# Kernel optimization log

Hardware: AMD Instinct MI355X
Metric: run time of the kernel (lower is better)

## Reference

```python
import jax, jax.numpy as jnp
import numpy as np

B, S, E, H = 8, 2048, 512, 4
D = E // H


def setup_inputs() -> dict:
    key = jax.random.key(0)
    ks = jax.random.split(key, 9)
    std = 0.05  # keras 'normal' initializer default stddev
    return {
        "x": jax.random.normal(ks[0], (B, S, E), dtype=jnp.float32),
        "Wq": jax.random.normal(ks[1], (E, E), dtype=jnp.float32) * std,
        "Wk": jax.random.normal(ks[2], (E, E), dtype=jnp.float32) * std,
        "Wv": jax.random.normal(ks[3], (E, E), dtype=jnp.float32) * std,
        "Wepi": jax.random.normal(ks[4], (S, S), dtype=jnp.float32) * std,
        "bq": jax.random.normal(ks[5], (S, 1), dtype=jnp.float32) * std,
        "bk": jax.random.normal(ks[6], (S, 1), dtype=jnp.float32) * std,
        "bv": jax.random.normal(ks[7], (S, 1), dtype=jnp.float32) * std,
        "bo": jax.random.normal(ks[8], (S, 1), dtype=jnp.float32) * std,
    }


def reference(x, Wq, Wk, Wv, Wepi, bq, bk, bv, bo):
    b, s, e = x.shape
    # QKV projections; [S,1] biases broadcast across the feature dim
    q = x @ Wq + bq  # [B,S,E]
    k = x @ Wk + bk
    v = x @ Wv + bv
    # split heads -> [B,H,S,D]
    q = q.reshape(b, s, H, D).transpose(0, 2, 1, 3)
    k = k.reshape(b, s, H, D).transpose(0, 2, 1, 3)
    v = v.reshape(b, s, H, D).transpose(0, 2, 1, 3)
    # NOTE: source scales by sqrt(seq_length), not sqrt(head_dim)
    scale = 1.0 / np.sqrt(float(s)).astype(np.float32)
    scores = jnp.einsum("bhsd,bhtd->bhst", q, k) * scale  # [B,H,S,S]
    attn = jax.nn.softmax(scores, axis=-1)
    # epigenomic multiplicative mask applied AFTER softmax (broadcast [S,S])
    attn = attn * Wepi
    effect = jnp.einsum("bhst,bhtd->bhsd", attn, v)  # [B,H,S,D]
    effect = effect.transpose(0, 2, 1, 3).reshape(b, s, e) + bo
    # original returns attention in merged-batch layout [B*H, S, S]
    return effect, attn.reshape(b * H, s, s)
```

## Files before the change

kernel.cpp:

```cpp
#include <hip/hip_runtime.h>
#include <hip/hip_bf16.h>

constexpr int Bn = 8, Sn = 2048, En = 512, Hn = 4, Dn = 128;
constexpr int BHn = Bn * Hn;
constexpr int Mqkv = Bn * Sn;

typedef __attribute__((ext_vector_type(8))) short short8;
typedef __attribute__((ext_vector_type(4))) float f32x4;

__device__ __forceinline__ unsigned short f2bf(float f) {
  unsigned int u = __builtin_bit_cast(unsigned int, f);
  u += 0x7FFF + ((u >> 16) & 1);
  return (unsigned short)(u >> 16);
}

__device__ __forceinline__ void bar_pub() {
  asm volatile("s_waitcnt lgkmcnt(0)" ::: "memory");
  __builtin_amdgcn_s_barrier();
  asm volatile("" ::: "memory");
}

__global__ __launch_bounds__(256) void qkv_kernel(
    const float* __restrict__ x, const float* __restrict__ Wq,
    const float* __restrict__ Wk, const float* __restrict__ Wv,
    const float* __restrict__ bq, const float* __restrict__ bk,
    const float* __restrict__ bv, unsigned short* __restrict__ qkv) {
  const int z = blockIdx.z;
  const float* W = (z == 0) ? Wq : (z == 1 ? Wk : Wv);
  const float* bias = (z == 0) ? bq : (z == 1 ? bk : bv);
  unsigned short* out = qkv + (size_t)z * BHn * Sn * Dn;

  __shared__ unsigned short As[128][40];
  __shared__ unsigned short BsT[128][40];

  const int t = threadIdx.x;
  const int l = t & 63, w = t >> 6;
  const int wm = w >> 1, wn = w & 1;
  const int m0 = blockIdx.x * 128, n0 = blockIdx.y * 128;

  f32x4 acc[4][4] = {};

  for (int k0 = 0; k0 < En; k0 += 32) {
    __syncthreads();
#pragma unroll
    for (int i = 0; i < 4; ++i) {
      int idx = t + i * 256;
      int row = idx >> 3, c4 = (idx & 7) * 4;
      float4 v = *reinterpret_cast<const float4*>(&x[(size_t)(m0 + row) * En + k0 + c4]);
      ushort4 p;
      p.x = f2bf(v.x); p.y = f2bf(v.y); p.z = f2bf(v.z); p.w = f2bf(v.w);
      *reinterpret_cast<ushort4*>(&As[row][c4]) = p;
    }
#pragma unroll
    for (int i = 0; i < 4; ++i) {
      int idx = t + i * 256;
      int kk = idx >> 5, c4 = (idx & 31) * 4;
      float4 v = *reinterpret_cast<const float4*>(&W[(size_t)(k0 + kk) * En + n0 + c4]);
      BsT[c4 + 0][kk] = f2bf(v.x);
      BsT[c4 + 1][kk] = f2bf(v.y);
      BsT[c4 + 2][kk] = f2bf(v.z);
      BsT[c4 + 3][kk] = f2bf(v.w);
    }
    __syncthreads();

    const int koff = (l >> 4) * 8;
    short8 a[4], bfr[4];
#pragma unroll
    for (int m = 0; m < 4; ++m)
      a[m] = *reinterpret_cast<const short8*>(&As[wm * 64 + m * 16 + (l & 15)][koff]);
#pragma unroll
    for (int n = 0; n < 4; ++n)
      bfr[n] = *reinterpret_cast<const short8*>(&BsT[wn * 64 + n * 16 + (l & 15)][koff]);
#pragma unroll
    for (int m = 0; m < 4; ++m)
#pragma unroll
      for (int n = 0; n < 4; ++n)
        acc[m][n] = __builtin_amdgcn_mfma_f32_16x16x32_bf16(a[m], bfr[n], acc[m][n], 0, 0, 0);
  }

#pragma unroll
  for (int m = 0; m < 4; ++m)
#pragma unroll
    for (int n = 0; n < 4; ++n)
#pragma unroll
      for (int j = 0; j < 4; ++j) {
        int row = m0 + wm * 64 + m * 16 + (l >> 4) * 4 + j;
        int col = n0 + wn * 64 + n * 16 + (l & 15);
        int s = row & (Sn - 1);
        float v = acc[m][n][j] + bias[s];
        int b = row >> 11;
        int h = col >> 7, d = col & 127;
        out[(size_t)((b * Hn + h) * Sn + s) * Dn + d] = f2bf(v);
      }
}

__global__ __launch_bounds__(256) void vtrans_kernel(
    const unsigned short* __restrict__ v, unsigned short* __restrict__ vT) {
  const int s0 = blockIdx.x * 64, d0 = blockIdx.y * 64;
  const int bh = blockIdx.z;
  const unsigned short* vp = v + (size_t)bh * Sn * Dn;
  unsigned short* op = vT + (size_t)bh * Dn * Sn;
  __shared__ unsigned short Ls[64][72];
  const int t = threadIdx.x;
#pragma unroll
  for (int it = 0; it < 2; ++it) {
    int flat = t + it * 256;
    int r = flat >> 3, cc = flat & 7;
    *reinterpret_cast<short8*>(&Ls[r][cc * 8]) =
        *reinterpret_cast<const short8*>(&vp[(size_t)(s0 + r) * Dn + d0 + cc * 8]);
  }
  __syncthreads();
#pragma unroll
  for (int it = 0; it < 2; ++it) {
    int flat = t + it * 256;
    int d = flat >> 3, sc = flat & 7;
    short8 o;
#pragma unroll
    for (int jo = 0; jo < 8; ++jo) {
      int jj = (jo + sc) & 7;
      o[jj] = (short)Ls[sc * 8 + jj][d];
    }
    *reinterpret_cast<short8*>(&op[(size_t)(d0 + d) * Sn + s0 + sc * 8]) = o;
  }
}

__global__ __launch_bounds__(256, 2) void fused_attn3_kernel(
    const unsigned short* __restrict__ qkv, const unsigned short* __restrict__ vT,
    const float* __restrict__ Wepi, const float* __restrict__ bo,
    float* __restrict__ attn, float* __restrict__ effect) {
  const int bh = blockIdx.y;
  const int s0 = blockIdx.x * 64;
  const unsigned short* qp = qkv + (size_t)bh * Sn * Dn;
  const unsigned short* kp = qkv + (size_t)(BHn + bh) * Sn * Dn;
  const unsigned short* vt = vT + (size_t)bh * Dn * Sn;

  __shared__ unsigned short Kb[2][64 * 128];
  __shared__ unsigned short Vt[128 * 64];
  __shared__ unsigned short Ps[64 * 64];

  const int t = threadIdx.x, l = t & 63, w = t >> 6;
  const int g = l >> 4, i = l & 15;
  const float scale = 0.022097086912079608f;

  short8 aq[4];
#pragma unroll
  for (int ks = 0; ks < 4; ++ks)
    aq[ks] = *reinterpret_cast<const short8*>(
        &qp[(size_t)(s0 + w * 16 + i) * Dn + ks * 32 + g * 8]);

  int ksrc[4], kdst[4], vsrc[4], vdst[4];
#pragma unroll
  for (int it = 0; it < 4; ++it) {
    int flat = t + it * 256;
    int r = flat >> 4, cc = flat & 15;
    ksrc[it] = r * Dn + cc * 8;
    kdst[it] = r * 128 + ((cc ^ (r & 15)) << 3);
    int d = flat >> 3, ct = flat & 7;
    vsrc[it] = d * Sn + ct * 8;
    vdst[it] = d * 64 + ((ct ^ (d & 7)) << 3);
  }

  short8 kreg[4];
#pragma unroll
  for (int it = 0; it < 4; ++it)
    kreg[it] = *reinterpret_cast<const short8*>(&kp[ksrc[it]]);
#pragma unroll
  for (int it = 0; it < 4; ++it)
    *reinterpret_cast<short8*>(&Kb[0][kdst[it]]) = kreg[it];
#pragma unroll
  for (int it = 0; it < 4; ++it)
    kreg[it] = *reinterpret_cast<const short8*>(&kp[(size_t)64 * Dn + ksrc[it]]);
  bar_pub();

  float rs[4] = {0.f, 0.f, 0.f, 0.f};

  for (int kt = 0; kt < 32; ++kt) {
    const int b = kt & 1;
    f32x4 acc[4] = {};
    __builtin_amdgcn_s_setprio(1);
#pragma unroll
    for (int ks = 0; ks < 4; ++ks)
#pragma unroll
      for (int nf = 0; nf < 4; ++nf) {
        short8 bk = *reinterpret_cast<const short8*>(
            &Kb[b][(nf * 16 + i) * 128 + (((ks * 4 + g) ^ i) << 3)]);
        acc[nf] = __builtin_amdgcn_mfma_f32_16x16x32_bf16(aq[ks], bk, acc[nf], 0, 0, 0);
      }
    __builtin_amdgcn_s_setprio(0);
#pragma unroll
    for (int j = 0; j < 4; ++j)
      rs[j] += __expf(acc[0][j] * scale) + __expf(acc[1][j] * scale) +
               __expf(acc[2][j] * scale) + __expf(acc[3][j] * scale);
    if (kt < 31) {
#pragma unroll
      for (int it = 0; it < 4; ++it)
        *reinterpret_cast<short8*>(&Kb[b ^ 1][kdst[it]]) = kreg[it];
      if (kt < 30)
#pragma unroll
        for (int it = 0; it < 4; ++it)
          kreg[it] = *reinterpret_cast<const short8*>(
              &kp[(size_t)(kt + 2) * 64 * Dn + ksrc[it]]);
    }
    bar_pub();
  }

  float rinv[4];
#pragma unroll
  for (int j = 0; j < 4; ++j) {
    float s = rs[j];
    s += __shfl_xor(s, 1); s += __shfl_xor(s, 2);
    s += __shfl_xor(s, 4); s += __shfl_xor(s, 8);
    rinv[j] = 1.0f / s;
  }

  short8 vreg[4];
#pragma unroll
  for (int it = 0; it < 4; ++it) {
    kreg[it] = *reinterpret_cast<const short8*>(&kp[ksrc[it]]);
    vreg[it] = *reinterpret_cast<const short8*>(&vt[vsrc[it]]);
  }
#pragma unroll
  for (int it = 0; it < 4; ++it) {
    *reinterpret_cast<short8*>(&Kb[0][kdst[it]]) = kreg[it];
    *reinterpret_cast<short8*>(&Vt[vdst[it]]) = vreg[it];
  }
#pragma unroll
  for (int it = 0; it < 4; ++it) {
    kreg[it] = *reinterpret_cast<const short8*>(&kp[(size_t)64 * Dn + ksrc[it]]);
    vreg[it] = *reinterpret_cast<const short8*>(&vt[64 + vsrc[it]]);
  }
  const float* wbase = Wepi + (size_t)(s0 + w * 16 + g * 4) * Sn + i;
  float wr[4][4];
#pragma unroll
  for (int nf = 0; nf < 4; ++nf)
#pragma unroll
    for (int j = 0; j < 4; ++j)
      wr[nf][j] = wbase[(size_t)j * Sn + nf * 16];
  bar_pub();

  f32x4 pv[8] = {};
  float* attn_bh = attn + (size_t)bh * Sn * Sn;

  for (int kt = 0; kt < 32; ++kt) {
    const int b = kt & 1;
    const int t0 = kt * 64;
    f32x4 acc[4] = {};
    __builtin_amdgcn_s_setprio(1);
#pragma unroll
    for (int ks = 0; ks < 4; ++ks)
#pragma unroll
      for (int nf = 0; nf < 4; ++nf) {
        short8 bk = *reinterpret_cast<const short8*>(
            &Kb[b][(nf * 16 + i) * 128 + (((ks * 4 + g) ^ i) << 3)]);
        acc[nf] = __builtin_amdgcn_mfma_f32_16x16x32_bf16(aq[ks], bk, acc[nf], 0, 0, 0);
      }
    __builtin_amdgcn_s_setprio(0);

#pragma unroll
    for (int nf = 0; nf < 4; ++nf)
#pragma unroll
      for (int j = 0; j < 4; ++j) {
        const int row = w * 16 + g * 4 + j;
        const int col = nf * 16 + i;
        float pf = __expf(acc[nf][j] * scale) * rinv[j] * wr[nf][j];
        attn_bh[(size_t)(s0 + row) * Sn + t0 + col] = pf;
        Ps[row * 64 + ((((nf * 2 + (i >> 3)) ^ (row & 7)) << 3) | (i & 7))] = f2bf(pf);
      }
    if (kt < 31)
#pragma unroll
      for (int nf = 0; nf < 4; ++nf)
#pragma unroll
        for (int j = 0; j < 4; ++j)
          wr[nf][j] = wbase[(size_t)j * Sn + t0 + 64 + nf * 16];
    if (kt < 31)
#pragma unroll
      for (int it = 0; it < 4; ++it)
        *reinterpret_cast<short8*>(&Kb[b ^ 1][kdst[it]]) = kreg[it];
    bar_pub();

    __builtin_amdgcn_s_setprio(1);
#pragma unroll
    for (int ks2 = 0; ks2 < 2; ++ks2) {
      short8 pa = *reinterpret_cast<const short8*>(
          &Ps[(w * 16 + i) * 64 + (((ks2 * 4 + g) ^ (i & 7)) << 3)]);
#pragma unroll
      for (int nf2 = 0; nf2 < 8; ++nf2) {
        const int d = nf2 * 16 + i;
        short8 bv = *reinterpret_cast<const short8*>(
            &Vt[d * 64 + (((ks2 * 4 + g) ^ (i & 7)) << 3)]);
        pv[nf2] = __builtin_amdgcn_mfma_f32_16x16x32_bf16(pa, bv, pv[nf2], 0, 0, 0);
      }
    }
    __builtin_amdgcn_s_setprio(0);
    bar_pub();

    if (kt < 31) {
#pragma unroll
      for (int it = 0; it < 4; ++it)
        *reinterpret_cast<short8*>(&Vt[vdst[it]]) = vreg[it];
      if (kt < 30)
#pragma unroll
        for (int it = 0; it < 4; ++it) {
          kreg[it] = *reinterpret_cast<const short8*>(
              &kp[(size_t)(t0 + 128) * Dn + ksrc[it]]);
          vreg[it] = *reinterpret_cast<const short8*>(&vt[t0 + 128 + vsrc[it]]);
        }
    }
  }

  const int b_ = bh >> 2, h_ = bh & 3;
#pragma unroll
  for (int j = 0; j < 4; ++j) {
    const int row = s0 + w * 16 + g * 4 + j;
    const float bias = bo[row];
#pragma unroll
    for (int nf2 = 0; nf2 < 8; ++nf2)
      effect[(size_t)(b_ * Sn + row) * En + h_ * Dn + nf2 * 16 + i] = pv[nf2][j] + bias;
  }
}

extern "C" void kernel_launch(void* const* d_in, const int* in_sizes, int n_in,
                              void* d_out, int out_size, void* d_ws, size_t ws_size,
                              hipStream_t stream) {
  const float* x    = (const float*)d_in[0];
  const float* Wq   = (const float*)d_in[1];
  const float* Wk   = (const float*)d_in[2];
  const float* Wv   = (const float*)d_in[3];
  const float* Wepi = (const float*)d_in[4];
  const float* bq   = (const float*)d_in[5];
  const float* bk   = (const float*)d_in[6];
  const float* bv   = (const float*)d_in[7];
  const float* bo   = (const float*)d_in[8];

  float* effect = (float*)d_out;
  float* attn = effect + (size_t)Bn * Sn * En;
  unsigned short* qkv = (unsigned short*)d_ws;
  unsigned short* vT = qkv + (size_t)3 * BHn * Sn * Dn;

  qkv_kernel<<<dim3(Mqkv / 128, En / 128, 3), 256, 0, stream>>>(x, Wq, Wk, Wv, bq, bk, bv, qkv);
  vtrans_kernel<<<dim3(Sn / 64, Dn / 64, BHn), 256, 0, stream>>>(
      qkv + (size_t)2 * BHn * Sn * Dn, vT);
  fused_attn3_kernel<<<dim3(Sn / 64, BHn), 256, 0, stream>>>(qkv, vT, Wepi, bo, attn, effect);
}
```

Before: 398.4 us.

## Transpose QK^T MFMA output for vectorized attn stores and per-wave P tiles

Swaps the MFMA operands so each lane holds four consecutive key columns of one query row. The attention probabilities and the Wepi mask can then be written and read as float4 instead of scalar strided accesses, and the row sum needs only two cross-lane shuffles. P is staged in a per-wave padded LDS tile, which removes one block barrier between the score and PV phases. V is double-buffered so the K/V refill and a single barrier sit at the end of each iteration. LDS use grows from the larger V buffer, which may affect the two-blocks-per-CU occupancy target.

```diff
diff --git a/kernel.cpp b/kernel.cpp
--- a/kernel.cpp
+++ b/kernel.cpp
@@ -124,7 +124,7 @@
   }
 }
 
-__global__ __launch_bounds__(256, 2) void fused_attn3_kernel(
+__global__ __launch_bounds__(256, 2) void fused_attn4_kernel(
     const unsigned short* __restrict__ qkv, const unsigned short* __restrict__ vT,
     const float* __restrict__ Wepi, const float* __restrict__ bo,
     float* __restrict__ attn, float* __restrict__ effect) {
@@ -135,8 +135,8 @@
   const unsigned short* vt = vT + (size_t)bh * Dn * Sn;
 
   __shared__ unsigned short Kb[2][64 * 128];
-  __shared__ unsigned short Vt[128 * 64];
-  __shared__ unsigned short Ps[64 * 64];
+  __shared__ unsigned short Vt[2][128 * 64];
+  __shared__ unsigned short Psw[4][16 * 72];
 
   const int t = threadIdx.x, l = t & 63, w = t >> 6;
   const int g = l >> 4, i = l & 15;
@@ -172,25 +172,27 @@
     kreg[it] = *reinterpret_cast<const short8*>(&kp[(size_t)64 * Dn + ksrc[it]]);
   bar_pub();
 
-  float rs[4] = {0.f, 0.f, 0.f, 0.f};
-
+  float rs = 0.f;
   for (int kt = 0; kt < 32; ++kt) {
     const int b = kt & 1;
-    f32x4 acc[4] = {};
+    f32x4 accT[4] = {};
     __builtin_amdgcn_s_setprio(1);
 #pragma unroll
     for (int ks = 0; ks < 4; ++ks)
 #pragma unroll
-      for (int nf = 0; nf < 4; ++nf) {
-        short8 bk = *reinterpret_cast<const short8*>(
-            &Kb[b][(nf * 16 + i) * 128 + (((ks * 4 + g) ^ i) << 3)]);
-        acc[nf] = __builtin_amdgcn_mfma_f32_16x16x32_bf16(aq[ks], bk, acc[nf], 0, 0, 0);
+      for (int tf = 0; tf < 4; ++tf) {
+        short8 ak = *reinterpret_cast<const short8*>(
+            &Kb[b][(tf * 16 + i) * 128 + (((ks * 4 + g) ^ i) << 3)]);
+        accT[tf] = __builtin_amdgcn_mfma_f32_16x16x32_bf16(ak, aq[ks], accT[tf], 0, 0, 0);
       }
     __builtin_amdgcn_s_setprio(0);
-#pragma unroll
-    for (int j = 0; j < 4; ++j)
-      rs[j] += __expf(acc[0][j] * scale) + __expf(acc[1][j] * scale) +
-               __expf(acc[2][j] * scale) + __expf(acc[3][j] * scale);
+    float p0 = 0.f, p1 = 0.f;
+#pragma unroll
+    for (int tf = 0; tf < 4; ++tf) {
+      p0 += __expf(accT[tf][0] * scale) + __expf(accT[tf][1] * scale);
+      p1 += __expf(accT[tf][2] * scale) + __expf(accT[tf][3] * scale);
+    }
+    rs += p0 + p1;
     if (kt < 31) {
 #pragma unroll
       for (int it = 0; it < 4; ++it)
@@ -203,15 +205,9 @@
     }
     bar_pub();
   }
-
-  float rinv[4];
-#pragma unroll
-  for (int j = 0; j < 4; ++j) {
-    float s = rs[j];
-    s += __shfl_xor(s, 1); s += __shfl_xor(s, 2);
-    s += __shfl_xor(s, 4); s += __shfl_xor(s, 8);
-    rinv[j] = 1.0f / s;
-  }
+  rs += __shfl_xor(rs, 16);
+  rs += __shfl_xor(rs, 32);
+  const float rinv = 1.0f / rs;
 
   short8 vreg[4];
 #pragma unroll
@@ -222,82 +218,77 @@
 #pragma unroll
   for (int it = 0; it < 4; ++it) {
     *reinterpret_cast<short8*>(&Kb[0][kdst[it]]) = kreg[it];
-    *reinterpret_cast<short8*>(&Vt[vdst[it]]) = vreg[it];
+    *reinterpret_cast<short8*>(&Vt[0][vdst[it]]) = vreg[it];
   }
 #pragma unroll
   for (int it = 0; it < 4; ++it) {
     kreg[it] = *reinterpret_cast<const short8*>(&kp[(size_t)64 * Dn + ksrc[it]]);
     vreg[it] = *reinterpret_cast<const short8*>(&vt[64 + vsrc[it]]);
   }
-  const float* wbase = Wepi + (size_t)(s0 + w * 16 + g * 4) * Sn + i;
-  float wr[4][4];
-#pragma unroll
-  for (int nf = 0; nf < 4; ++nf)
-#pragma unroll
-    for (int j = 0; j < 4; ++j)
-      wr[nf][j] = wbase[(size_t)j * Sn + nf * 16];
+  const float* wrow = Wepi + (size_t)(s0 + w * 16 + i) * Sn + g * 4;
+  float4 wr[4];
+#pragma unroll
+  for (int tf = 0; tf < 4; ++tf)
+    wr[tf] = *reinterpret_cast<const float4*>(&wrow[tf * 16]);
   bar_pub();
 
   f32x4 pv[8] = {};
-  float* attn_bh = attn + (size_t)bh * Sn * Sn;
+  float* arow = attn + (size_t)bh * Sn * Sn + (size_t)(s0 + w * 16 + i) * Sn;
 
   for (int kt = 0; kt < 32; ++kt) {
     const int b = kt & 1;
     const int t0 = kt * 64;
-    f32x4 acc[4] = {};
+    f32x4 accT[4] = {};
     __builtin_amdgcn_s_setprio(1);
 #pragma unroll
     for (int ks = 0; ks < 4; ++ks)
 #pragma unroll
-      for (int nf = 0; nf < 4; ++nf) {
-        short8 bk = *reinterpret_cast<const short8*>(
-            &Kb[b][(nf * 16 + i) * 128 + (((ks * 4 + g) ^ i) << 3)]);
-        acc[nf] = __builtin_amdgcn_mfma_f32_16x16x32_bf16(aq[ks], bk, acc[nf], 0, 0, 0);
+      for (int tf = 0; tf < 4; ++tf) {
+        short8 ak = *reinterpret_cast<const short8*>(
+            &Kb[b][(tf * 16 + i) * 128 + (((ks * 4 + g) ^ i) << 3)]);
+        accT[tf] = __builtin_amdgcn_mfma_f32_16x16x32_bf16(ak, aq[ks], accT[tf], 0, 0, 0);
       }
     __builtin_amdgcn_s_setprio(0);
 
-#pragma unroll
-    for (int nf = 0; nf < 4; ++nf)
-#pragma unroll
-      for (int j = 0; j < 4; ++j) {
-        const int row = w * 16 + g * 4 + j;
-        const int col = nf * 16 + i;
-        float pf = __expf(acc[nf][j] * scale) * rinv[j] * wr[nf][j];
-        attn_bh[(size_t)(s0 + row) * Sn + t0 + col] = pf;
-        Ps[row * 64 + ((((nf * 2 + (i >> 3)) ^ (row & 7)) << 3) | (i & 7))] = f2bf(pf);
-      }
+    float4 nwr[4];
     if (kt < 31)
 #pragma unroll
-      for (int nf = 0; nf < 4; ++nf)
-#pragma unroll
-        for (int j = 0; j < 4; ++j)
-          wr[nf][j] = wbase[(size_t)j * Sn + t0 + 64 + nf * 16];
-    if (kt < 31)
-#pragma unroll
-      for (int it = 0; it < 4; ++it)
+      for (int tf = 0; tf < 4; ++tf)
+        nwr[tf] = *reinterpret_cast<const float4*>(&wrow[t0 + 64 + tf * 16]);
+
+#pragma unroll
+    for (int tf = 0; tf < 4; ++tf) {
+      float q0 = __expf(accT[tf][0] * scale) * rinv * wr[tf].x;
+      float q1 = __expf(accT[tf][1] * scale) * rinv * wr[tf].y;
+      float q2 = __expf(accT[tf][2] * scale) * rinv * wr[tf].z;
+      float q3 = __expf(accT[tf][3] * scale) * rinv * wr[tf].w;
+      float4 pf4 = {q0, q1, q2, q3};
+      *reinterpret_cast<float4*>(&arow[t0 + tf * 16 + g * 4]) = pf4;
+      ushort4 pk;
+      pk.x = f2bf(q0); pk.y = f2bf(q1); pk.z = f2bf(q2); pk.w = f2bf(q3);
+      *reinterpret_cast<ushort4*>(&Psw[w][i * 72 + tf * 16 + g * 4]) = pk;
+    }
+
+    __builtin_amdgcn_s_setprio(1);
+#pragma unroll
+    for (int ks2 = 0; ks2 < 2; ++ks2) {
+      short8 pa = *reinterpret_cast<const short8*>(&Psw[w][i * 72 + ks2 * 32 + g * 8]);
+#pragma unroll
+      for (int df = 0; df < 8; ++df) {
+        const int d = df * 16 + i;
+        short8 bv = *reinterpret_cast<const short8*>(
+            &Vt[b][d * 64 + (((ks2 * 4 + g) ^ (d & 7)) << 3)]);
+        pv[df] = __builtin_amdgcn_mfma_f32_16x16x32_bf16(pa, bv, pv[df], 0, 0, 0);
+      }
+    }
+    __builtin_amdgcn_s_setprio(0);
+
+    if (kt < 31) {
+#pragma unroll
+      for (int it = 0; it < 4; ++it) {
         *reinterpret_cast<short8*>(&Kb[b ^ 1][kdst[it]]) = kreg[it];
-    bar_pub();
-
-    __builtin_amdgcn_s_setprio(1);
-#pragma unroll
-    for (int ks2 = 0; ks2 < 2; ++ks2) {
-      short8 pa = *reinterpret_cast<const short8*>(
-          &Ps[(w * 16 + i) * 64 + (((ks2 * 4 + g) ^ (i & 7)) << 3)]);
-#pragma unroll
-      for (int nf2 = 0; nf2 < 8; ++nf2) {
-        const int d = nf2 * 16 + i;
-        short8 bv = *reinterpret_cast<const short8*>(
-            &Vt[d * 64 + (((ks2 * 4 + g) ^ (i & 7)) << 3)]);
-        pv[nf2] = __builtin_amdgcn_mfma_f32_16x16x32_bf16(pa, bv, pv[nf2], 0, 0, 0);
-      }
-    }
-    __builtin_amdgcn_s_setprio(0);
-    bar_pub();
-
-    if (kt < 31) {
-#pragma unroll
-      for (int it = 0; it < 4; ++it)
-        *reinterpret_cast<short8*>(&Vt[vdst[it]]) = vreg[it];
+        *reinterpret_cast<short8*>(&Vt[b ^ 1][vdst[it]]) = vreg[it];
+      }
       if (kt < 30)
 #pragma unroll
         for (int it = 0; it < 4; ++it) {
@@ -305,7 +296,10 @@
               &kp[(size_t)(t0 + 128) * Dn + ksrc[it]]);
           vreg[it] = *reinterpret_cast<const short8*>(&vt[t0 + 128 + vsrc[it]]);
         }
-    }
+#pragma unroll
+      for (int tf = 0; tf < 4; ++tf) wr[tf] = nwr[tf];
+    }
+    bar_pub();
   }
 
   const int b_ = bh >> 2, h_ = bh & 3;
@@ -314,8 +308,8 @@
     const int row = s0 + w * 16 + g * 4 + j;
     const float bias = bo[row];
 #pragma unroll
-    for (int nf2 = 0; nf2 < 8; ++nf2)
-      effect[(size_t)(b_ * Sn + row) * En + h_ * Dn + nf2 * 16 + i] = pv[nf2][j] + bias;
+    for (int df = 0; df < 8; ++df)
+      effect[(size_t)(b_ * Sn + row) * En + h_ * Dn + df * 16 + i] = pv[df][j] + bias;
   }
 }
 
@@ -340,5 +334,5 @@
   qkv_kernel<<<dim3(Mqkv / 128, En / 128, 3), 256, 0, stream>>>(x, Wq, Wk, Wv, bq, bk, bv, qkv);
   vtrans_kernel<<<dim3(Sn / 64, Dn / 64, BHn), 256, 0, stream>>>(
       qkv + (size_t)2 * BHn * Sn * Dn, vT);
-  fused_attn3_kernel<<<dim3(Sn / 64, BHn), 256, 0, stream>>>(qkv, vT, Wepi, bo, attn, effect);
-}
+  fused_attn4_kernel<<<dim3(Sn / 64, BHn), 256, 0, stream>>>(qkv, vT, Wepi, bo, attn, effect);
+}
```

After: 411.1 us. +3.2%, slower.
